# Optimization experiments

Hardware: AMD Instinct MI355X
Metric: run time of the kernel (lower is better)

## Reference

```python
import jax, jax.numpy as jnp
import numpy as np

B, T, D, H = 8, 512, 1024, 16
DH = D // H
MAX_LEN = 512  # max_pos_encoding


def rel_pos_encoding(seq_len, dim):
    # Relative sinusoidal PE, full (non-causal) context, no hidden state.
    # positions: max_len-1 ... 1, 0, -1 ... -(max_len-1)
    pos = jnp.concatenate([
        jnp.arange(MAX_LEN - 1, 0, -1, dtype=jnp.float32),
        jnp.arange(0, -MAX_LEN, -1, dtype=jnp.float32),
    ])  # (2*max_len-1,)
    inv_freq = jnp.power(10000.0, -2.0 * jnp.arange(dim // 2, dtype=jnp.float32) / dim)
    ang = pos[:, None] * inv_freq[None, :]  # (2M-1, D/2)
    pe = jnp.zeros((2 * MAX_LEN - 1, dim), dtype=jnp.float32)
    pe = pe.at[:, 0::2].set(jnp.sin(ang)).at[:, 1::2].set(jnp.cos(ang))
    # non-causal slice: [max_len - seq_len : max_len - 1 + seq_len] -> 2T-1 rows
    return pe[MAX_LEN - seq_len: MAX_LEN - 1 + seq_len]


def rel_to_abs(s):
    # full-context skewing (Bello et al.): s is (B, H, T1, T2) with T2 = 2*T1 - 1
    b, h, t1, t2 = s.shape
    s = jnp.pad(s, ((0, 0), (0, 0), (0, 0), (0, 1)))
    s = s.reshape(b, h, t1 * (t2 + 1))
    s = jnp.pad(s, ((0, 0), (0, 0), (0, t2 - t1)))
    s = s.reshape(b, h, t1 + 1, t2)
    return s[:, :, :t1, t1 - 1:]  # (B, H, T1, T1)


def setup_inputs() -> dict:
    key = jax.random.key(0)
    ks = jax.random.split(key, 9)
    sc = 1.0 / np.sqrt(D)
    return {
        "x": jax.random.normal(ks[0], (B, T, D), dtype=jnp.float32),
        "Wq": jax.random.normal(ks[1], (D, D), dtype=jnp.float32) * sc,
        "bq": jnp.zeros((D,), dtype=jnp.float32),
        "Wk": jax.random.normal(ks[2], (D, D), dtype=jnp.float32) * sc,
        "bk": jnp.zeros((D,), dtype=jnp.float32),
        "Wv": jax.random.normal(ks[3], (D, D), dtype=jnp.float32) * sc,
        "bv": jnp.zeros((D,), dtype=jnp.float32),
        "Wp": jax.random.normal(ks[4], (D, D), dtype=jnp.float32) * sc,
        "bp": jnp.zeros((D,), dtype=jnp.float32),
        "Wo": jax.random.normal(ks[5], (D, D), dtype=jnp.float32) * sc,
        "bo": jnp.zeros((D,), dtype=jnp.float32),
        "u": jax.random.normal(ks[6], (D,), dtype=jnp.float32) * 0.02,
        "v": jax.random.normal(ks[7], (D,), dtype=jnp.float32) * 0.02,
    }


def reference(x, Wq, bq, Wk, bk, Wv, bv, Wp, bp, Wo, bo, u, v):
    b, t, d = x.shape
    Q = x @ Wq.T + bq
    K = x @ Wk.T + bk
    V = x @ Wv.T + bv
    Qu = Q + u
    Qv = Q + v
    # relative positional embeddings, projected: (2T-1, D)
    E = rel_pos_encoding(t, d) @ Wp.T + bp
    # split heads
    Qu = Qu.reshape(b, t, H, DH).transpose(0, 2, 1, 3)  # (B,H,T,dh)
    Qv = Qv.reshape(b, t, H, DH).transpose(0, 2, 1, 3)
    Kh = K.reshape(b, t, H, DH).transpose(0, 2, 1, 3)
    Vh = V.reshape(b, t, H, DH).transpose(0, 2, 1, 3)
    Eh = E.reshape(2 * t - 1, H, DH)  # (R,H,dh)
    att_scores_K = jnp.einsum("bhqd,bhkd->bhqk", Qu, Kh)
    att_scores_E = rel_to_abs(jnp.einsum("bhqd,rhd->bhqr", Qv, Eh))
    att_scores = (att_scores_K + att_scores_E) / jnp.sqrt(jnp.float32(DH))
    att_w = jax.nn.softmax(att_scores, axis=-1)
    O = jnp.einsum("bhqk,bhkd->bhqd", att_w, Vh)
    O = O.transpose(0, 2, 1, 3).reshape(b, t, d)
    return O @ Wo.T + bo
```

## Files before the change

kernel.cpp:

```cpp
#include <hip/hip_runtime.h>
#include <hip/hip_bf16.h>
#include <cmath>

using short8  = __attribute__((ext_vector_type(8))) short;
using f32x4   = __attribute__((ext_vector_type(4))) float;
using uint4v  = __attribute__((ext_vector_type(4))) unsigned;

#define DEV static __device__ __forceinline__

DEV unsigned short f2bf(float f) {
  union { float f; unsigned u; } v; v.f = f;
  unsigned r = v.u + 0x7FFFu + ((v.u >> 16) & 1u);
  return (unsigned short)(r >> 16);
}
DEV float bf2f(unsigned short b) {
  union { unsigned u; float f; } v; v.u = ((unsigned)b) << 16;
  return v.f;
}

DEV void async_copy16(const void* g, void* l) {
  __builtin_amdgcn_global_load_lds(
      (const __attribute__((address_space(1))) void*)g,
      (__attribute__((address_space(3))) void*)l, 16, 0, 0);
}

#define DPPF(x, ctrl)                                                     \
  __builtin_bit_cast(float, __builtin_amdgcn_update_dpp(                  \
      __builtin_bit_cast(int, (x)), __builtin_bit_cast(int, (x)), (ctrl), \
      0xF, 0xF, false))

DEV float rowmax16(float t) {
  t = fmaxf(t, DPPF(t, 0x128));
  t = fmaxf(t, DPPF(t, 0x124));
  t = fmaxf(t, DPPF(t, 0x122));
  t = fmaxf(t, DPPF(t, 0x121));
  return t;
}
DEV float rowsum16(float t) {
  t += DPPF(t, 0x128);
  t += DPPF(t, 0x124);
  t += DPPF(t, 0x122);
  t += DPPF(t, 0x121);
  return t;
}
DEV unsigned dpp_xor8(unsigned x) {
  return (unsigned)__builtin_amdgcn_update_dpp((int)x, (int)x, 0x128, 0xF, 0xF, false);
}

DEV void load_ehalf(const unsigned short* __restrict__ E, char* sE, int h,
                    int H, int slot, int wave, int lane) {
#pragma unroll
  for (int it = 0; it < 2; ++it) {
    const unsigned o = (unsigned)(it * 4096 + wave * 1024 + lane * 16);
    const unsigned row = o >> 7;
    const unsigned x = (o & 127u) ^ ((row & 7u) << 4);
    async_copy16(E + (size_t)(H * 64 + (int)row) * 1024 + h * 64 + (x >> 1),
                 sE + slot * 8192 + it * 4096 + wave * 1024);
  }
}

__global__ __launch_bounds__(256) void prep_kernel(
    const float* __restrict__ x,  const float* __restrict__ Wq,
    const float* __restrict__ Wk, const float* __restrict__ Wv,
    const float* __restrict__ Wp, const float* __restrict__ Wo,
    const float* __restrict__ bq, const float* __restrict__ bk,
    const float* __restrict__ bv,
    unsigned short* __restrict__ xb, unsigned short* __restrict__ Wqkvb,
    unsigned short* __restrict__ Wpb, unsigned short* __restrict__ Wob,
    unsigned short* __restrict__ peb, float* __restrict__ bqkv) {
  const int blk = blockIdx.x;
  const int tid = threadIdx.x;
  if (blk < 9216) {
    const float* src;
    unsigned short* dst;
    int i;
    if (blk < 4096) {
      src = x; dst = xb; i = blk * 256 + tid;
    } else {
      const int w = (blk - 4096) >> 10;
      i = ((blk - 4096) & 1023) * 256 + tid;
      if      (w == 0) { src = Wq; dst = Wqkvb; }
      else if (w == 1) { src = Wk; dst = Wqkvb + 1048576; }
      else if (w == 2) { src = Wv; dst = Wqkvb + 2097152; }
      else if (w == 3) { src = Wp; dst = Wpb; }
      else             { src = Wo; dst = Wob; }
    }
    float4 v = ((const float4*)src)[i];
    ushort4 o;
    o.x = f2bf(v.x); o.y = f2bf(v.y); o.z = f2bf(v.z); o.w = f2bf(v.w);
    ((ushort4*)dst)[i] = o;
  } else if (blk < 11264) {
    const int idx = (blk - 9216) * 256 + tid;
    const int r = idx >> 9;
    const int m = idx & 511;
    const float inv_freq = __expf((float)m * -0.017988946039016004f);
    const float ang = (float)(511 - r) * inv_freq;
    peb[(size_t)r * 1024 + 2 * m]     = f2bf(sinf(ang));
    peb[(size_t)r * 1024 + 2 * m + 1] = f2bf(cosf(ang));
  } else {
    const int i = (blk - 11264) * 256 + tid;
    const float* s = (i < 1024) ? bq : (i < 2048) ? bk : bv;
    bqkv[i] = s[i & 1023];
  }
}

template <int OUTF32>
DEV void gemm_tile(const unsigned short* __restrict__ A,
                   const unsigned short* __restrict__ B,
                   const float* __restrict__ bias, void* __restrict__ Cout,
                   int N, int K, int m0, int n0, int tid,
                   unsigned short* sA, unsigned short* sB) {
  const int lane = tid & 63;
  const int wave = tid >> 6;

  const unsigned short* gA[4];
  const unsigned short* gB[4];
  unsigned ldst[4];
#pragma unroll
  for (int it = 0; it < 4; ++it) {
    unsigned o = (unsigned)(it * 4096 + wave * 1024 + lane * 16);
    unsigned row = o >> 7;
    unsigned x = (o & 127u) ^ ((row & 7u) << 4);
    ldst[it] = it * 4096 + wave * 1024;
    gA[it] = A + (size_t)(m0 + (int)row) * K + (x >> 1);
    gB[it] = B + (size_t)(n0 + (int)row) * K + (x >> 1);
  }

  f32x4 acc[4][4];
#pragma unroll
  for (int i = 0; i < 4; ++i)
#pragma unroll
    for (int j = 0; j < 4; ++j) acc[i][j] = f32x4{0.f, 0.f, 0.f, 0.f};

  const int wm = (wave >> 1) << 6;
  const int wn = (wave & 1) << 6;
  const int rsel = lane & 15;
  const int ksel = (lane >> 4) << 4;

  for (int k0 = 0; k0 < K; k0 += 64) {
#pragma unroll
    for (int it = 0; it < 4; ++it) {
      async_copy16(gA[it] + k0, (char*)sA + ldst[it]);
      async_copy16(gB[it] + k0, (char*)sB + ldst[it]);
    }
    __syncthreads();
#pragma unroll
    for (int kb = 0; kb < 2; ++kb) {
      const int kbyte = kb * 64 + ksel;
      short8 af[4], bf8[4];
#pragma unroll
      for (int i = 0; i < 4; ++i) {
        const int ra = wm + i * 16 + rsel;
        af[i] = *(const short8*)((const char*)sA + ra * 128 + (kbyte ^ ((ra & 7) << 4)));
        const int rb = wn + i * 16 + rsel;
        bf8[i] = *(const short8*)((const char*)sB + rb * 128 + (kbyte ^ ((rb & 7) << 4)));
      }
#pragma unroll
      for (int i = 0; i < 4; ++i)
#pragma unroll
        for (int j = 0; j < 4; ++j)
          acc[i][j] = __builtin_amdgcn_mfma_f32_16x16x32_bf16(af[i], bf8[j], acc[i][j], 0, 0, 0);
    }
    __syncthreads();
  }

#pragma unroll
  for (int i = 0; i < 4; ++i) {
    const int row0 = m0 + wm + i * 16 + ((lane >> 4) << 2);
#pragma unroll
    for (int j = 0; j < 4; ++j) {
      const int col = n0 + wn + j * 16 + rsel;
      const float bb = bias[col];
#pragma unroll
      for (int r = 0; r < 4; ++r) {
        const float val = acc[i][j][r] + bb;
        if (OUTF32)
          ((float*)Cout)[(size_t)(row0 + r) * N + col] = val;
        else
          ((unsigned short*)Cout)[(size_t)(row0 + r) * N + col] = f2bf(val);
      }
    }
  }
}

__global__ __launch_bounds__(256) void gemm_qkv_e_kernel(
    const unsigned short* __restrict__ xb, const unsigned short* __restrict__ Wqkvb,
    const float* __restrict__ bqkv, unsigned short* __restrict__ QKVb,
    const unsigned short* __restrict__ peb, const unsigned short* __restrict__ Wpb,
    const float* __restrict__ bp, unsigned short* __restrict__ Eb) {
  __shared__ unsigned short sA[128 * 64];
  __shared__ unsigned short sB[128 * 64];
  const int cpx = 104;
  const int bid = (blockIdx.x & 7) * cpx + (blockIdx.x >> 3);
  if (bid < 768) {
    const int mt = bid / 24, nt = bid - mt * 24;
    gemm_tile<0>(xb, Wqkvb, bqkv, QKVb, 3072, 1024, mt << 7, nt << 7,
                 threadIdx.x, sA, sB);
  } else {
    const int b2 = bid - 768;
    gemm_tile<0>(peb, Wpb, bp, Eb, 1024, 1024, (b2 >> 3) << 7, (b2 & 7) << 7,
                 threadIdx.x, sA, sB);
  }
}

__global__ __launch_bounds__(256) void gemm_out_kernel(
    const unsigned short* __restrict__ Ob, const unsigned short* __restrict__ Wob,
    const float* __restrict__ bo, float* __restrict__ out) {
  __shared__ unsigned short sA[128 * 64];
  __shared__ unsigned short sB[128 * 64];
  const int cpx = 32;
  const int bid = (blockIdx.x & 7) * cpx + (blockIdx.x >> 3);
  gemm_tile<1>(Ob, Wob, bo, out, 1024, 1024, (bid >> 3) << 7, (bid & 7) << 7,
               threadIdx.x, sA, sB);
}

__global__ __launch_bounds__(256, 2) void attn_kernel(
    const unsigned short* __restrict__ QKV,
    const unsigned short* __restrict__ E,
    const float* __restrict__ uvec, const float* __restrict__ vvec,
    unsigned short* __restrict__ O) {
  __shared__ unsigned short sK[2 * 4096];
  __shared__ unsigned short sE[3 * 4096];
  __shared__ unsigned short sVt[2 * 4096];
  __shared__ unsigned short sP[4][1024];

  const int tid = threadIdx.x;
  const int lane = tid & 63;
  const int wave = tid >> 6;
  const int cpx = gridDim.x >> 3;
  const int bid = (blockIdx.x & 7) * cpx + (blockIdx.x >> 3);
  const int qt = bid & 7;
  const int h = (bid >> 3) & 15;
  const int b = bid >> 7;
  const int q0 = qt << 6;

  const int rsel = lane & 15;
  const int g = lane >> 4;
  const int ilocb = g << 2;
  const int c0w = 48 - wave * 16;

  const unsigned short* Qb = QKV + (size_t)b * 512 * 3072 + h * 64;
  const unsigned short* Kb = Qb + 1024;
  const unsigned short* Vb = Qb + 2048;

  const float sc = 0.125f * 1.44269504088896f;

  short8 v8b[2];
#pragma unroll
  for (int it = 0; it < 2; ++it) {
    const int c = it * 256 + tid;
    v8b[it] = *(const short8*)(Vb + (size_t)(c >> 3) * 3072 + ((c & 7) << 3));
  }
#pragma unroll
  for (int it = 0; it < 2; ++it) {
    const unsigned o = (unsigned)(it * 4096 + wave * 1024 + lane * 16);
    const unsigned row = o >> 7;
    const unsigned x = (o & 127u) ^ ((row & 7u) << 4);
    async_copy16(Kb + (size_t)row * 3072 + (x >> 1),
                 (char*)sK + it * 4096 + wave * 1024);
  }
  load_ehalf(E, (char*)sE, h, 7 - qt, (7 - qt) % 3, wave, lane);
  load_ehalf(E, (char*)sE, h, 8 - qt, (8 - qt) % 3, wave, lane);

  short8 aU[2], aV[2];
  {
    const int qrow = q0 + wave * 16 + rsel;
    const int dob = g * 8;
#pragma unroll
    for (int kb = 0; kb < 2; ++kb) {
      short8 q8 = *(const short8*)(Qb + (size_t)qrow * 3072 + kb * 32 + dob);
#pragma unroll
      for (int j = 0; j < 8; ++j) {
        const float qf = bf2f((unsigned short)q8[j]);
        aU[kb][j] = (short)f2bf((qf + uvec[h * 64 + kb * 32 + dob + j]) * sc);
        aV[kb][j] = (short)f2bf((qf + vvec[h * 64 + kb * 32 + dob + j]) * sc);
      }
    }
  }

  {
#pragma unroll
    for (int it = 0; it < 2; ++it) {
      const int c = it * 256 + tid;
      const int trow = c >> 3;
      const int db = (c & 7) << 3;
      const int odd = trow & 1;
      const int kp = (trow & ~1) * 2;
      const uint4v dw = __builtin_bit_cast(uint4v, v8b[it]);
#pragma unroll
      for (int p = 0; p < 4; ++p) {
        const unsigned mine = dw[p];
        const unsigned other = dpp_xor8(mine);
        const unsigned res = odd ? ((mine & 0xffff0000u) | (other >> 16))
                                 : ((other << 16) | (mine & 0xffffu));
        const int d = db + 2 * p + odd;
        *(unsigned*)((char*)sVt + d * 128 +
                     (kp ^ (((d ^ (d >> 3)) & 7) << 4))) = res;
      }
    }
  }
#pragma unroll
  for (int it = 0; it < 2; ++it) {
    const int c = it * 256 + tid;
    v8b[it] = *(const short8*)(Vb + (size_t)(64 + (c >> 3)) * 3072 + ((c & 7) << 3));
  }

  int srcLn[4];
  bool hiSel[4];
#pragma unroll
  for (int r = 0; r < 4; ++r) {
    const int offs = 15 - (ilocb + r) + rsel;
    srcLn[r] = (lane & 48) | (offs & 15);
    hiSel[r] = offs >= 16;
  }

  float mrun[4], lrun[4];
  f32x4 oacc[4];
#pragma unroll
  for (int r = 0; r < 4; ++r) { mrun[r] = -INFINITY; lrun[r] = 0.f; }
#pragma unroll
  for (int n = 0; n < 4; ++n) oacc[n] = f32x4{0.f, 0.f, 0.f, 0.f};

  for (int kt = 0; kt < 8; ++kt) {
    const int k0 = kt << 6;
    const int cur = kt & 1;
    const int H0 = 7 - qt + kt;
    const int slotLo = H0 % 3;
    const int slotHi = (H0 + 1) % 3;

    __syncthreads();

    if (kt < 7) {
      const int kn = k0 + 64;
#pragma unroll
      for (int it = 0; it < 2; ++it) {
        const unsigned o = (unsigned)(it * 4096 + wave * 1024 + lane * 16);
        const unsigned row = o >> 7;
        const unsigned x = (o & 127u) ^ ((row & 7u) << 4);
        async_copy16(Kb + (size_t)(kn + (int)row) * 3072 + (x >> 1),
                     (char*)sK + (cur ^ 1) * 8192 + it * 4096 + wave * 1024);
      }
      load_ehalf(E, (char*)sE, h, H0 + 2, (H0 + 2) % 3, wave, lane);
#pragma unroll
      for (int it = 0; it < 2; ++it) {
        const int c = it * 256 + tid;
        const int trow = c >> 3;
        const int db = (c & 7) << 3;
        const int odd = trow & 1;
        const int kp = (trow & ~1) * 2;
        const uint4v dw = __builtin_bit_cast(uint4v, v8b[it]);
#pragma unroll
        for (int p = 0; p < 4; ++p) {
          const unsigned mine = dw[p];
          const unsigned other = dpp_xor8(mine);
          const unsigned res = odd ? ((mine & 0xffff0000u) | (other >> 16))
                                   : ((other << 16) | (mine & 0xffffu));
          const int d = db + 2 * p + odd;
          *(unsigned*)((char*)sVt + (cur ^ 1) * 8192 + d * 128 +
                       (kp ^ (((d ^ (d >> 3)) & 7) << 4))) = res;
        }
      }
      if (kt < 6) {
#pragma unroll
        for (int it = 0; it < 2; ++it) {
          const int c = it * 256 + tid;
          v8b[it] = *(const short8*)(Vb + (size_t)(kn + 64 + (c >> 3)) * 3072 +
                                     ((c & 7) << 3));
        }
      }
    }

    f32x4 skacc[4], gacc[5];
#pragma unroll
    for (int nf = 0; nf < 4; ++nf) skacc[nf] = f32x4{0.f, 0.f, 0.f, 0.f};
#pragma unroll
    for (int cf = 0; cf < 5; ++cf) gacc[cf] = f32x4{0.f, 0.f, 0.f, 0.f};
    __builtin_amdgcn_s_setprio(1);
#pragma unroll
    for (int kb = 0; kb < 2; ++kb) {
      const int kbyte = kb * 64 + g * 16;
#pragma unroll
      for (int nf = 0; nf < 4; ++nf) {
        const int rb = nf * 16 + rsel;
        short8 b8 = *(const short8*)((const char*)sK + cur * 8192 + rb * 128 +
                                     (kbyte ^ ((rb & 7) << 4)));
        skacc[nf] = __builtin_amdgcn_mfma_f32_16x16x32_bf16(aU[kb], b8, skacc[nf], 0, 0, 0);
      }
#pragma unroll
      for (int cf = 0; cf < 5; ++cf) {
        const int rowbase = c0w + cf * 16;
        const int rb = rowbase + rsel;
        const int slot = (rowbase >> 6) ? slotHi : slotLo;
        short8 e8 = *(const short8*)((const char*)sE + slot * 8192 +
                                     (rb & 63) * 128 + (kbyte ^ ((rb & 7) << 4)));
        gacc[cf] = __builtin_amdgcn_mfma_f32_16x16x32_bf16(aV[kb], e8, gacc[cf], 0, 0, 0);
      }
    }
    __builtin_amdgcn_s_setprio(0);

#pragma unroll
    for (int r = 0; r < 4; ++r) {
      float gsh[5];
#pragma unroll
      for (int cf = 0; cf < 5; ++cf) gsh[cf] = __shfl(gacc[cf][r], srcLn[r], 64);
#pragma unroll
      for (int nf = 0; nf < 4; ++nf)
        skacc[nf][r] += hiSel[r] ? gsh[nf + 1] : gsh[nf];
    }

    float scl[4], rsum[4];
#pragma unroll
    for (int r = 0; r < 4; ++r) {
      float t = fmaxf(fmaxf(skacc[0][r], skacc[1][r]), fmaxf(skacc[2][r], skacc[3][r]));
      t = rowmax16(t);
      const float mnew = fmaxf(mrun[r], t);
      scl[r] = __builtin_amdgcn_exp2f(mrun[r] - mnew);
      mrun[r] = mnew;
      rsum[r] = 0.f;
    }
#pragma unroll
    for (int nf = 0; nf < 4; ++nf)
#pragma unroll
      for (int r = 0; r < 4; ++r) {
        const float p = __builtin_amdgcn_exp2f(skacc[nf][r] - mrun[r]);
        rsum[r] += p;
        const int iloc = ilocb + r;
        const int jb = (nf * 16 + rsel) * 2;
        *(unsigned short*)((char*)sP[wave] + iloc * 128 + (jb ^ ((iloc & 7) << 4))) = f2bf(p);
      }
#pragma unroll
    for (int r = 0; r < 4; ++r)
      lrun[r] = lrun[r] * scl[r] + rowsum16(rsum[r]);
#pragma unroll
    for (int nf = 0; nf < 4; ++nf)
#pragma unroll
      for (int r = 0; r < 4; ++r) oacc[nf][r] *= scl[r];

    __builtin_amdgcn_s_setprio(1);
#pragma unroll
    for (int kb = 0; kb < 2; ++kb) {
      const int kbyte = kb * 64 + g * 16;
      short8 ap = *(const short8*)((const char*)sP[wave] + rsel * 128 +
                                   (kbyte ^ ((rsel & 7) << 4)));
#pragma unroll
      for (int nf = 0; nf < 4; ++nf) {
        const int rv = nf * 16 + rsel;
        short8 vb8 = *(const short8*)((const char*)sVt + cur * 8192 + rv * 128 +
                                      (kbyte ^ (((rv ^ (rv >> 3)) & 7) << 4)));
        oacc[nf] = __builtin_amdgcn_mfma_f32_16x16x32_bf16(ap, vb8, oacc[nf], 0, 0, 0);
      }
    }
    __builtin_amdgcn_s_setprio(0);
  }

#pragma unroll
  for (int nf = 0; nf < 4; ++nf) {
#pragma unroll
    for (int r = 0; r < 4; ++r) {
      const int t = q0 + wave * 16 + ilocb + r;
      const int col = h * 64 + nf * 16 + rsel;
      O[(size_t)(b * 512 + t) * 1024 + col] = f2bf(oacc[nf][r] / lrun[r]);
    }
  }
}

extern "C" void kernel_launch(void* const* d_in, const int* in_sizes, int n_in,
                              void* d_out, int out_size, void* d_ws, size_t ws_size,
                              hipStream_t stream) {
  const float* x  = (const float*)d_in[0];
  const float* Wq = (const float*)d_in[1];
  const float* bq = (const float*)d_in[2];
  const float* Wk = (const float*)d_in[3];
  const float* bk = (const float*)d_in[4];
  const float* Wv = (const float*)d_in[5];
  const float* bv = (const float*)d_in[6];
  const float* Wp = (const float*)d_in[7];
  const float* bp = (const float*)d_in[8];
  const float* Wo = (const float*)d_in[9];
  const float* bo = (const float*)d_in[10];
  const float* u  = (const float*)d_in[11];
  const float* v  = (const float*)d_in[12];
  float* out = (float*)d_out;

  char* ws = (char*)d_ws;
  const size_t MB = 1024 * 1024;
  unsigned short* xb    = (unsigned short*)(ws);
  unsigned short* Wqkvb = (unsigned short*)(ws + 8 * MB);
  unsigned short* Wpb   = (unsigned short*)(ws + 14 * MB);
  unsigned short* Wob   = (unsigned short*)(ws + 16 * MB);
  unsigned short* peb   = (unsigned short*)(ws + 18 * MB);
  unsigned short* QKVb  = (unsigned short*)(ws + 20 * MB);
  unsigned short* Eb    = (unsigned short*)(ws + 44 * MB);
  unsigned short* Ob    = (unsigned short*)(ws + 46 * MB);
  float* bqkv           = (float*)(ws + 54 * MB);

  prep_kernel<<<dim3(11276), dim3(256), 0, stream>>>(
      x, Wq, Wk, Wv, Wp, Wo, bq, bk, bv, xb, Wqkvb, Wpb, Wob, peb, bqkv);

  gemm_qkv_e_kernel<<<dim3(832), dim3(256), 0, stream>>>(
      xb, Wqkvb, bqkv, QKVb, peb, Wpb, bp, Eb);
  attn_kernel<<<dim3(1024), dim3(256), 0, stream>>>(QKVb, Eb, u, v, Ob);
  gemm_out_kernel<<<dim3(256), dim3(256), 0, stream>>>(Ob, Wob, bo, out);
}
```

Baseline: 120.9 us.

## Double attention query tile to 128 rows with 8 waves sharing K/V/E tiles

The attention kernel now uses 512-thread blocks covering 128 query rows (8 waves of 16 rows) instead of 64. Each staged K, transposed V and E tile in shared memory is reused by twice as many waves, and per-thread load work halves. The E ring buffer grows to 4 slots indexed by H&3, and the grid halves to 512 blocks. Fewer blocks and larger shared memory per block may reduce occupancy and load balance across CUs, and the launch bound asks for 4 blocks of 512 threads, which limits registers per thread.

```diff
diff --git a/kernel.cpp b/kernel.cpp
--- a/kernel.cpp
+++ b/kernel.cpp
@@ -45,18 +45,6 @@
 }
 DEV unsigned dpp_xor8(unsigned x) {
   return (unsigned)__builtin_amdgcn_update_dpp((int)x, (int)x, 0x128, 0xF, 0xF, false);
-}
-
-DEV void load_ehalf(const unsigned short* __restrict__ E, char* sE, int h,
-                    int H, int slot, int wave, int lane) {
-#pragma unroll
-  for (int it = 0; it < 2; ++it) {
-    const unsigned o = (unsigned)(it * 4096 + wave * 1024 + lane * 16);
-    const unsigned row = o >> 7;
-    const unsigned x = (o & 127u) ^ ((row & 7u) << 4);
-    async_copy16(E + (size_t)(H * 64 + (int)row) * 1024 + h * 64 + (x >> 1),
-                 sE + slot * 8192 + it * 4096 + wave * 1024);
-  }
 }
 
 __global__ __launch_bounds__(256) void prep_kernel(
@@ -214,30 +202,30 @@
                threadIdx.x, sA, sB);
 }
 
-__global__ __launch_bounds__(256, 2) void attn_kernel(
+__global__ __launch_bounds__(512, 4) void attn_kernel(
     const unsigned short* __restrict__ QKV,
     const unsigned short* __restrict__ E,
     const float* __restrict__ uvec, const float* __restrict__ vvec,
     unsigned short* __restrict__ O) {
   __shared__ unsigned short sK[2 * 4096];
-  __shared__ unsigned short sE[3 * 4096];
+  __shared__ unsigned short sE[4 * 4096];
   __shared__ unsigned short sVt[2 * 4096];
-  __shared__ unsigned short sP[4][1024];
+  __shared__ unsigned short sP[8][1024];
 
   const int tid = threadIdx.x;
   const int lane = tid & 63;
   const int wave = tid >> 6;
   const int cpx = gridDim.x >> 3;
   const int bid = (blockIdx.x & 7) * cpx + (blockIdx.x >> 3);
-  const int qt = bid & 7;
-  const int h = (bid >> 3) & 15;
-  const int b = bid >> 7;
-  const int q0 = qt << 6;
+  const int qt = bid & 3;
+  const int h = (bid >> 2) & 15;
+  const int b = bid >> 6;
+  const int q0 = qt << 7;
 
   const int rsel = lane & 15;
   const int g = lane >> 4;
   const int ilocb = g << 2;
-  const int c0w = 48 - wave * 16;
+  const int c0w = 112 - wave * 16;
 
   const unsigned short* Qb = QKV + (size_t)b * 512 * 3072 + h * 64;
   const unsigned short* Kb = Qb + 1024;
@@ -245,22 +233,24 @@
 
   const float sc = 0.125f * 1.44269504088896f;
 
-  short8 v8b[2];
-#pragma unroll
-  for (int it = 0; it < 2; ++it) {
-    const int c = it * 256 + tid;
-    v8b[it] = *(const short8*)(Vb + (size_t)(c >> 3) * 3072 + ((c & 7) << 3));
-  }
-#pragma unroll
-  for (int it = 0; it < 2; ++it) {
-    const unsigned o = (unsigned)(it * 4096 + wave * 1024 + lane * 16);
+  short8 v8b;
+  v8b = *(const short8*)(Vb + (size_t)(tid >> 3) * 3072 + ((tid & 7) << 3));
+
+  {
+    const unsigned o = (unsigned)(wave * 1024 + lane * 16);
     const unsigned row = o >> 7;
     const unsigned x = (o & 127u) ^ ((row & 7u) << 4);
-    async_copy16(Kb + (size_t)row * 3072 + (x >> 1),
-                 (char*)sK + it * 4096 + wave * 1024);
-  }
-  load_ehalf(E, (char*)sE, h, 7 - qt, (7 - qt) % 3, wave, lane);
-  load_ehalf(E, (char*)sE, h, 8 - qt, (8 - qt) % 3, wave, lane);
+    async_copy16(Kb + (size_t)row * 3072 + (x >> 1), (char*)sK + wave * 1024);
+  }
+#pragma unroll
+  for (int hh = 0; hh < 3; ++hh) {
+    const int H = 6 - 2 * qt + hh;
+    const unsigned o = (unsigned)(wave * 1024 + lane * 16);
+    const unsigned row = o >> 7;
+    const unsigned x = (o & 127u) ^ ((row & 7u) << 4);
+    async_copy16(E + (size_t)(H * 64 + (int)row) * 1024 + h * 64 + (x >> 1),
+                 (char*)sE + (H & 3) * 8192 + wave * 1024);
+  }
 
   short8 aU[2], aV[2];
   {
@@ -279,31 +269,22 @@
   }
 
   {
-#pragma unroll
-    for (int it = 0; it < 2; ++it) {
-      const int c = it * 256 + tid;
-      const int trow = c >> 3;
-      const int db = (c & 7) << 3;
-      const int odd = trow & 1;
-      const int kp = (trow & ~1) * 2;
-      const uint4v dw = __builtin_bit_cast(uint4v, v8b[it]);
-#pragma unroll
-      for (int p = 0; p < 4; ++p) {
-        const unsigned mine = dw[p];
-        const unsigned other = dpp_xor8(mine);
-        const unsigned res = odd ? ((mine & 0xffff0000u) | (other >> 16))
-                                 : ((other << 16) | (mine & 0xffffu));
-        const int d = db + 2 * p + odd;
-        *(unsigned*)((char*)sVt + d * 128 +
-                     (kp ^ (((d ^ (d >> 3)) & 7) << 4))) = res;
-      }
-    }
-  }
-#pragma unroll
-  for (int it = 0; it < 2; ++it) {
-    const int c = it * 256 + tid;
-    v8b[it] = *(const short8*)(Vb + (size_t)(64 + (c >> 3)) * 3072 + ((c & 7) << 3));
-  }
+    const int trow = tid >> 3;
+    const int db = (tid & 7) << 3;
+    const int odd = trow & 1;
+    const int kp = (trow & ~1) * 2;
+    const uint4v dw = __builtin_bit_cast(uint4v, v8b);
+#pragma unroll
+    for (int p = 0; p < 4; ++p) {
+      const unsigned mine = dw[p];
+      const unsigned other = dpp_xor8(mine);
+      const unsigned res = odd ? ((mine & 0xffff0000u) | (other >> 16))
+                               : ((other << 16) | (mine & 0xffffu));
+      const int d = db + 2 * p + odd;
+      *(unsigned*)((char*)sVt + d * 128 + (kp ^ (((d ^ (d >> 3)) & 7) << 4))) = res;
+    }
+  }
+  v8b = *(const short8*)(Vb + (size_t)(64 + (tid >> 3)) * 3072 + ((tid & 7) << 3));
 
   int srcLn[4];
   bool hiSel[4];
@@ -324,31 +305,33 @@
   for (int kt = 0; kt < 8; ++kt) {
     const int k0 = kt << 6;
     const int cur = kt & 1;
-    const int H0 = 7 - qt + kt;
-    const int slotLo = H0 % 3;
-    const int slotHi = (H0 + 1) % 3;
+    const int H0 = 6 - 2 * qt + kt;
 
     __syncthreads();
 
     if (kt < 7) {
       const int kn = k0 + 64;
-#pragma unroll
-      for (int it = 0; it < 2; ++it) {
-        const unsigned o = (unsigned)(it * 4096 + wave * 1024 + lane * 16);
+      {
+        const unsigned o = (unsigned)(wave * 1024 + lane * 16);
         const unsigned row = o >> 7;
         const unsigned x = (o & 127u) ^ ((row & 7u) << 4);
         async_copy16(Kb + (size_t)(kn + (int)row) * 3072 + (x >> 1),
-                     (char*)sK + (cur ^ 1) * 8192 + it * 4096 + wave * 1024);
-      }
-      load_ehalf(E, (char*)sE, h, H0 + 2, (H0 + 2) % 3, wave, lane);
-#pragma unroll
-      for (int it = 0; it < 2; ++it) {
-        const int c = it * 256 + tid;
-        const int trow = c >> 3;
-        const int db = (c & 7) << 3;
+                     (char*)sK + (cur ^ 1) * 8192 + wave * 1024);
+      }
+      {
+        const int H = H0 + 3;
+        const unsigned o = (unsigned)(wave * 1024 + lane * 16);
+        const unsigned row = o >> 7;
+        const unsigned x = (o & 127u) ^ ((row & 7u) << 4);
+        async_copy16(E + (size_t)(H * 64 + (int)row) * 1024 + h * 64 + (x >> 1),
+                     (char*)sE + (H & 3) * 8192 + wave * 1024);
+      }
+      {
+        const int trow = tid >> 3;
+        const int db = (tid & 7) << 3;
         const int odd = trow & 1;
         const int kp = (trow & ~1) * 2;
-        const uint4v dw = __builtin_bit_cast(uint4v, v8b[it]);
+        const uint4v dw = __builtin_bit_cast(uint4v, v8b);
 #pragma unroll
         for (int p = 0; p < 4; ++p) {
           const unsigned mine = dw[p];
@@ -360,14 +343,9 @@
                        (kp ^ (((d ^ (d >> 3)) & 7) << 4))) = res;
         }
       }
-      if (kt < 6) {
-#pragma unroll
-        for (int it = 0; it < 2; ++it) {
-          const int c = it * 256 + tid;
-          v8b[it] = *(const short8*)(Vb + (size_t)(kn + 64 + (c >> 3)) * 3072 +
-                                     ((c & 7) << 3));
-        }
-      }
+      if (kt < 6)
+        v8b = *(const short8*)(Vb + (size_t)(kn + 64 + (tid >> 3)) * 3072 +
+                               ((tid & 7) << 3));
     }
 
     f32x4 skacc[4], gacc[5];
@@ -390,7 +368,7 @@
       for (int cf = 0; cf < 5; ++cf) {
         const int rowbase = c0w + cf * 16;
         const int rb = rowbase + rsel;
-        const int slot = (rowbase >> 6) ? slotHi : slotLo;
+        const int slot = (H0 + (rowbase >> 6)) & 3;
         short8 e8 = *(const short8*)((const char*)sE + slot * 8192 +
                                      (rb & 63) * 128 + (kbyte ^ ((rb & 7) << 4)));
         gacc[cf] = __builtin_amdgcn_mfma_f32_16x16x32_bf16(aV[kb], e8, gacc[cf], 0, 0, 0);
@@ -499,6 +477,6 @@
 
   gemm_qkv_e_kernel<<<dim3(832), dim3(256), 0, stream>>>(
       xb, Wqkvb, bqkv, QKVb, peb, Wpb, bp, Eb);
-  attn_kernel<<<dim3(1024), dim3(256), 0, stream>>>(QKVb, Eb, u, v, Ob);
+  attn_kernel<<<dim3(512), dim3(512), 0, stream>>>(QKVb, Eb, u, v, Ob);
   gemm_out_kernel<<<dim3(256), dim3(256), 0, stream>>>(Ob, Wob, bo, out);
 }
```

Result: slower. 135.5 us (+12.1%).

## Double attention query tile to 128 rows per block, reusing K/E/V fragments

Applied to the files above, without the earlier changes.

Each attention block now handles 128 query rows, with each wave owning two 16-row fragments instead of one, and the grid halves to 512 blocks. K, V and relative-position E fragments loaded from LDS are reused across both fragments, and the E window grows to a 4-slot ring holding 3 tiles plus a prefetch. This cuts redundant K/V/E global and LDS traffic per query row, at the cost of more registers, more LDS per block, and fewer blocks to spread across the CUs.

```diff
diff --git a/kernel.cpp b/kernel.cpp
--- a/kernel.cpp
+++ b/kernel.cpp
@@ -45,18 +45,6 @@
 }
 DEV unsigned dpp_xor8(unsigned x) {
   return (unsigned)__builtin_amdgcn_update_dpp((int)x, (int)x, 0x128, 0xF, 0xF, false);
-}
-
-DEV void load_ehalf(const unsigned short* __restrict__ E, char* sE, int h,
-                    int H, int slot, int wave, int lane) {
-#pragma unroll
-  for (int it = 0; it < 2; ++it) {
-    const unsigned o = (unsigned)(it * 4096 + wave * 1024 + lane * 16);
-    const unsigned row = o >> 7;
-    const unsigned x = (o & 127u) ^ ((row & 7u) << 4);
-    async_copy16(E + (size_t)(H * 64 + (int)row) * 1024 + h * 64 + (x >> 1),
-                 sE + slot * 8192 + it * 4096 + wave * 1024);
-  }
 }
 
 __global__ __launch_bounds__(256) void prep_kernel(
@@ -220,24 +208,24 @@
     const float* __restrict__ uvec, const float* __restrict__ vvec,
     unsigned short* __restrict__ O) {
   __shared__ unsigned short sK[2 * 4096];
-  __shared__ unsigned short sE[3 * 4096];
+  __shared__ unsigned short sE[4 * 4096];
   __shared__ unsigned short sVt[2 * 4096];
-  __shared__ unsigned short sP[4][1024];
+  __shared__ unsigned short sP[4][2048];
 
   const int tid = threadIdx.x;
   const int lane = tid & 63;
   const int wave = tid >> 6;
   const int cpx = gridDim.x >> 3;
   const int bid = (blockIdx.x & 7) * cpx + (blockIdx.x >> 3);
-  const int qt = bid & 7;
-  const int h = (bid >> 3) & 15;
-  const int b = bid >> 7;
-  const int q0 = qt << 6;
+  const int qt = bid & 3;
+  const int h = (bid >> 2) & 15;
+  const int b = bid >> 6;
+  const int q0 = qt << 7;
 
   const int rsel = lane & 15;
   const int g = lane >> 4;
   const int ilocb = g << 2;
-  const int c0w = 48 - wave * 16;
+  const int cb0 = 96 - 32 * wave;
 
   const unsigned short* Qb = QKV + (size_t)b * 512 * 3072 + h * 64;
   const unsigned short* Kb = Qb + 1024;
@@ -259,12 +247,23 @@
     async_copy16(Kb + (size_t)row * 3072 + (x >> 1),
                  (char*)sK + it * 4096 + wave * 1024);
   }
-  load_ehalf(E, (char*)sE, h, 7 - qt, (7 - qt) % 3, wave, lane);
-  load_ehalf(E, (char*)sE, h, 8 - qt, (8 - qt) % 3, wave, lane);
-
-  short8 aU[2], aV[2];
-  {
-    const int qrow = q0 + wave * 16 + rsel;
+#pragma unroll
+  for (int hh = 0; hh < 3; ++hh) {
+    const int H = 6 - 2 * qt + hh;
+#pragma unroll
+    for (int it = 0; it < 2; ++it) {
+      const unsigned o = (unsigned)(it * 4096 + wave * 1024 + lane * 16);
+      const unsigned row = o >> 7;
+      const unsigned x = (o & 127u) ^ ((row & 7u) << 4);
+      async_copy16(E + (size_t)(H * 64 + (int)row) * 1024 + h * 64 + (x >> 1),
+                   (char*)sE + (H & 3) * 8192 + it * 4096 + wave * 1024);
+    }
+  }
+
+  short8 aU[2][2], aV[2][2];
+#pragma unroll
+  for (int f = 0; f < 2; ++f) {
+    const int qrow = q0 + 32 * wave + 16 * f + rsel;
     const int dob = g * 8;
 #pragma unroll
     for (int kb = 0; kb < 2; ++kb) {
@@ -272,31 +271,28 @@
 #pragma unroll
       for (int j = 0; j < 8; ++j) {
         const float qf = bf2f((unsigned short)q8[j]);
-        aU[kb][j] = (short)f2bf((qf + uvec[h * 64 + kb * 32 + dob + j]) * sc);
-        aV[kb][j] = (short)f2bf((qf + vvec[h * 64 + kb * 32 + dob + j]) * sc);
-      }
-    }
-  }
-
-  {
-#pragma unroll
-    for (int it = 0; it < 2; ++it) {
-      const int c = it * 256 + tid;
-      const int trow = c >> 3;
-      const int db = (c & 7) << 3;
-      const int odd = trow & 1;
-      const int kp = (trow & ~1) * 2;
-      const uint4v dw = __builtin_bit_cast(uint4v, v8b[it]);
-#pragma unroll
-      for (int p = 0; p < 4; ++p) {
-        const unsigned mine = dw[p];
-        const unsigned other = dpp_xor8(mine);
-        const unsigned res = odd ? ((mine & 0xffff0000u) | (other >> 16))
-                                 : ((other << 16) | (mine & 0xffffu));
-        const int d = db + 2 * p + odd;
-        *(unsigned*)((char*)sVt + d * 128 +
-                     (kp ^ (((d ^ (d >> 3)) & 7) << 4))) = res;
-      }
+        aU[f][kb][j] = (short)f2bf((qf + uvec[h * 64 + kb * 32 + dob + j]) * sc);
+        aV[f][kb][j] = (short)f2bf((qf + vvec[h * 64 + kb * 32 + dob + j]) * sc);
+      }
+    }
+  }
+
+#pragma unroll
+  for (int it = 0; it < 2; ++it) {
+    const int c = it * 256 + tid;
+    const int trow = c >> 3;
+    const int db = (c & 7) << 3;
+    const int odd = trow & 1;
+    const int kp = (trow & ~1) * 2;
+    const uint4v dw = __builtin_bit_cast(uint4v, v8b[it]);
+#pragma unroll
+    for (int p = 0; p < 4; ++p) {
+      const unsigned mine = dw[p];
+      const unsigned other = dpp_xor8(mine);
+      const unsigned res = odd ? ((mine & 0xffff0000u) | (other >> 16))
+                               : ((other << 16) | (mine & 0xffffu));
+      const int d = db + 2 * p + odd;
+      *(unsigned*)((char*)sVt + d * 128 + (kp ^ (((d ^ (d >> 3)) & 7) << 4))) = res;
     }
   }
 #pragma unroll
@@ -314,19 +310,21 @@
     hiSel[r] = offs >= 16;
   }
 
-  float mrun[4], lrun[4];
-  f32x4 oacc[4];
-#pragma unroll
-  for (int r = 0; r < 4; ++r) { mrun[r] = -INFINITY; lrun[r] = 0.f; }
-#pragma unroll
-  for (int n = 0; n < 4; ++n) oacc[n] = f32x4{0.f, 0.f, 0.f, 0.f};
+  float mrun[2][4], lrun[2][4];
+  f32x4 oacc[2][4];
+#pragma unroll
+  for (int f = 0; f < 2; ++f)
+#pragma unroll
+    for (int r = 0; r < 4; ++r) { mrun[f][r] = -INFINITY; lrun[f][r] = 0.f; }
+#pragma unroll
+  for (int f = 0; f < 2; ++f)
+#pragma unroll
+    for (int n = 0; n < 4; ++n) oacc[f][n] = f32x4{0.f, 0.f, 0.f, 0.f};
 
   for (int kt = 0; kt < 8; ++kt) {
     const int k0 = kt << 6;
     const int cur = kt & 1;
-    const int H0 = 7 - qt + kt;
-    const int slotLo = H0 % 3;
-    const int slotHi = (H0 + 1) % 3;
+    const int H0 = 6 - 2 * qt + kt;
 
     __syncthreads();
 
@@ -340,7 +338,17 @@
         async_copy16(Kb + (size_t)(kn + (int)row) * 3072 + (x >> 1),
                      (char*)sK + (cur ^ 1) * 8192 + it * 4096 + wave * 1024);
       }
-      load_ehalf(E, (char*)sE, h, H0 + 2, (H0 + 2) % 3, wave, lane);
+      {
+        const int H = H0 + 3;
+#pragma unroll
+        for (int it = 0; it < 2; ++it) {
+          const unsigned o = (unsigned)(it * 4096 + wave * 1024 + lane * 16);
+          const unsigned row = o >> 7;
+          const unsigned x = (o & 127u) ^ ((row & 7u) << 4);
+          async_copy16(E + (size_t)(H * 64 + (int)row) * 1024 + h * 64 + (x >> 1),
+                       (char*)sE + (H & 3) * 8192 + it * 4096 + wave * 1024);
+        }
+      }
 #pragma unroll
       for (int it = 0; it < 2; ++it) {
         const int c = it * 256 + tid;
@@ -370,98 +378,131 @@
       }
     }
 
-    f32x4 skacc[4], gacc[5];
-#pragma unroll
-    for (int nf = 0; nf < 4; ++nf) skacc[nf] = f32x4{0.f, 0.f, 0.f, 0.f};
-#pragma unroll
-    for (int cf = 0; cf < 5; ++cf) gacc[cf] = f32x4{0.f, 0.f, 0.f, 0.f};
+    f32x4 skacc[2][4], gacc[2][5];
+#pragma unroll
+    for (int f = 0; f < 2; ++f) {
+#pragma unroll
+      for (int nf = 0; nf < 4; ++nf) skacc[f][nf] = f32x4{0.f, 0.f, 0.f, 0.f};
+#pragma unroll
+      for (int cf = 0; cf < 5; ++cf) gacc[f][cf] = f32x4{0.f, 0.f, 0.f, 0.f};
+    }
     __builtin_amdgcn_s_setprio(1);
 #pragma unroll
     for (int kb = 0; kb < 2; ++kb) {
       const int kbyte = kb * 64 + g * 16;
+      short8 kb8[4];
 #pragma unroll
       for (int nf = 0; nf < 4; ++nf) {
         const int rb = nf * 16 + rsel;
-        short8 b8 = *(const short8*)((const char*)sK + cur * 8192 + rb * 128 +
-                                     (kbyte ^ ((rb & 7) << 4)));
-        skacc[nf] = __builtin_amdgcn_mfma_f32_16x16x32_bf16(aU[kb], b8, skacc[nf], 0, 0, 0);
-      }
-#pragma unroll
-      for (int cf = 0; cf < 5; ++cf) {
-        const int rowbase = c0w + cf * 16;
+        kb8[nf] = *(const short8*)((const char*)sK + cur * 8192 + rb * 128 +
+                                   (kbyte ^ ((rb & 7) << 4)));
+      }
+#pragma unroll
+      for (int f = 0; f < 2; ++f)
+#pragma unroll
+        for (int nf = 0; nf < 4; ++nf)
+          skacc[f][nf] = __builtin_amdgcn_mfma_f32_16x16x32_bf16(
+              aU[f][kb], kb8[nf], skacc[f][nf], 0, 0, 0);
+      short8 eb8[6];
+#pragma unroll
+      for (int cfu = 0; cfu < 6; ++cfu) {
+        const int rowbase = cb0 + 16 * cfu;
         const int rb = rowbase + rsel;
-        const int slot = (rowbase >> 6) ? slotHi : slotLo;
-        short8 e8 = *(const short8*)((const char*)sE + slot * 8192 +
-                                     (rb & 63) * 128 + (kbyte ^ ((rb & 7) << 4)));
-        gacc[cf] = __builtin_amdgcn_mfma_f32_16x16x32_bf16(aV[kb], e8, gacc[cf], 0, 0, 0);
-      }
+        const int slot = (H0 + (rowbase >> 6)) & 3;
+        eb8[cfu] = *(const short8*)((const char*)sE + slot * 8192 +
+                                    (rb & 63) * 128 + (kbyte ^ ((rb & 7) << 4)));
+      }
+#pragma unroll
+      for (int f = 0; f < 2; ++f)
+#pragma unroll
+        for (int j = 0; j < 5; ++j)
+          gacc[f][j] = __builtin_amdgcn_mfma_f32_16x16x32_bf16(
+              aV[f][kb], eb8[j + 1 - f], gacc[f][j], 0, 0, 0);
     }
     __builtin_amdgcn_s_setprio(0);
 
 #pragma unroll
-    for (int r = 0; r < 4; ++r) {
-      float gsh[5];
-#pragma unroll
-      for (int cf = 0; cf < 5; ++cf) gsh[cf] = __shfl(gacc[cf][r], srcLn[r], 64);
+    for (int f = 0; f < 2; ++f)
+#pragma unroll
+      for (int r = 0; r < 4; ++r) {
+        float gsh[5];
+#pragma unroll
+        for (int cf = 0; cf < 5; ++cf)
+          gsh[cf] = __shfl(gacc[f][cf][r], srcLn[r], 64);
+#pragma unroll
+        for (int nf = 0; nf < 4; ++nf)
+          skacc[f][nf][r] += hiSel[r] ? gsh[nf + 1] : gsh[nf];
+      }
+
+    float scl[2][4];
+#pragma unroll
+    for (int f = 0; f < 2; ++f) {
+      float rsum[4];
+#pragma unroll
+      for (int r = 0; r < 4; ++r) {
+        float t = fmaxf(fmaxf(skacc[f][0][r], skacc[f][1][r]),
+                        fmaxf(skacc[f][2][r], skacc[f][3][r]));
+        t = rowmax16(t);
+        const float mnew = fmaxf(mrun[f][r], t);
+        scl[f][r] = __builtin_amdgcn_exp2f(mrun[f][r] - mnew);
+        mrun[f][r] = mnew;
+        rsum[r] = 0.f;
+      }
 #pragma unroll
       for (int nf = 0; nf < 4; ++nf)
-        skacc[nf][r] += hiSel[r] ? gsh[nf + 1] : gsh[nf];
-    }
-
-    float scl[4], rsum[4];
-#pragma unroll
-    for (int r = 0; r < 4; ++r) {
-      float t = fmaxf(fmaxf(skacc[0][r], skacc[1][r]), fmaxf(skacc[2][r], skacc[3][r]));
-      t = rowmax16(t);
-      const float mnew = fmaxf(mrun[r], t);
-      scl[r] = __builtin_amdgcn_exp2f(mrun[r] - mnew);
-      mrun[r] = mnew;
-      rsum[r] = 0.f;
-    }
-#pragma unroll
-    for (int nf = 0; nf < 4; ++nf)
-#pragma unroll
-      for (int r = 0; r < 4; ++r) {
-        const float p = __builtin_amdgcn_exp2f(skacc[nf][r] - mrun[r]);
-        rsum[r] += p;
-        const int iloc = ilocb + r;
-        const int jb = (nf * 16 + rsel) * 2;
-        *(unsigned short*)((char*)sP[wave] + iloc * 128 + (jb ^ ((iloc & 7) << 4))) = f2bf(p);
-      }
-#pragma unroll
-    for (int r = 0; r < 4; ++r)
-      lrun[r] = lrun[r] * scl[r] + rowsum16(rsum[r]);
-#pragma unroll
-    for (int nf = 0; nf < 4; ++nf)
-#pragma unroll
-      for (int r = 0; r < 4; ++r) oacc[nf][r] *= scl[r];
+#pragma unroll
+        for (int r = 0; r < 4; ++r) {
+          const float p = __builtin_amdgcn_exp2f(skacc[f][nf][r] - mrun[f][r]);
+          rsum[r] += p;
+          const int rloc = 16 * f + ilocb + r;
+          const int jb = (nf * 16 + rsel) * 2;
+          *(unsigned short*)((char*)sP[wave] + rloc * 128 +
+                             (jb ^ ((rloc & 7) << 4))) = f2bf(p);
+        }
+#pragma unroll
+      for (int r = 0; r < 4; ++r)
+        lrun[f][r] = lrun[f][r] * scl[f][r] + rowsum16(rsum[r]);
+#pragma unroll
+      for (int nf = 0; nf < 4; ++nf)
+#pragma unroll
+        for (int r = 0; r < 4; ++r) oacc[f][nf][r] *= scl[f][r];
+    }
 
     __builtin_amdgcn_s_setprio(1);
 #pragma unroll
     for (int kb = 0; kb < 2; ++kb) {
       const int kbyte = kb * 64 + g * 16;
-      short8 ap = *(const short8*)((const char*)sP[wave] + rsel * 128 +
-                                   (kbyte ^ ((rsel & 7) << 4)));
+      short8 ap[2];
+#pragma unroll
+      for (int f = 0; f < 2; ++f) {
+        const int pr = 16 * f + rsel;
+        ap[f] = *(const short8*)((const char*)sP[wave] + pr * 128 +
+                                 (kbyte ^ ((pr & 7) << 4)));
+      }
 #pragma unroll
       for (int nf = 0; nf < 4; ++nf) {
         const int rv = nf * 16 + rsel;
         short8 vb8 = *(const short8*)((const char*)sVt + cur * 8192 + rv * 128 +
                                       (kbyte ^ (((rv ^ (rv >> 3)) & 7) << 4)));
-        oacc[nf] = __builtin_amdgcn_mfma_f32_16x16x32_bf16(ap, vb8, oacc[nf], 0, 0, 0);
+#pragma unroll
+        for (int f = 0; f < 2; ++f)
+          oacc[f][nf] = __builtin_amdgcn_mfma_f32_16x16x32_bf16(
+              ap[f], vb8, oacc[f][nf], 0, 0, 0);
       }
     }
     __builtin_amdgcn_s_setprio(0);
   }
 
 #pragma unroll
-  for (int nf = 0; nf < 4; ++nf) {
-#pragma unroll
-    for (int r = 0; r < 4; ++r) {
-      const int t = q0 + wave * 16 + ilocb + r;
-      const int col = h * 64 + nf * 16 + rsel;
-      O[(size_t)(b * 512 + t) * 1024 + col] = f2bf(oacc[nf][r] / lrun[r]);
-    }
-  }
+  for (int f = 0; f < 2; ++f)
+#pragma unroll
+    for (int nf = 0; nf < 4; ++nf)
+#pragma unroll
+      for (int r = 0; r < 4; ++r) {
+        const int t = q0 + 32 * wave + 16 * f + ilocb + r;
+        const int col = h * 64 + nf * 16 + rsel;
+        O[(size_t)(b * 512 + t) * 1024 + col] = f2bf(oacc[f][nf][r] / lrun[f][r]);
+      }
 }
 
 extern "C" void kernel_launch(void* const* d_in, const int* in_sizes, int n_in,
@@ -499,6 +540,6 @@
 
   gemm_qkv_e_kernel<<<dim3(832), dim3(256), 0, stream>>>(
       xb, Wqkvb, bqkv, QKVb, peb, Wpb, bp, Eb);
-  attn_kernel<<<dim3(1024), dim3(256), 0, stream>>>(QKVb, Eb, u, v, Ob);
+  attn_kernel<<<dim3(512), dim3(256), 0, stream>>>(QKVb, Eb, u, v, Ob);
   gemm_out_kernel<<<dim3(256), dim3(256), 0, stream>>>(Ob, Wob, bo, out);
 }
```

After: 121.0 us. Within noise of the previous version (+0.1%).
